# Kernel optimization log

Measured on AMD Instinct MI355X. Metric: run time of the kernel, lower is better.

The kernel has to match this reference:

```python
import jax, jax.numpy as jnp
import numpy as np

B, L, H, V = 256, 2048, 64, 64


def setup_inputs() -> dict:
    key = jax.random.key(0)
    ks = jax.random.split(key, 16)
    s = 0.05
    return {
        "seq": jax.random.randint(ks[0], (B, L), 0, V),
        "embed": jax.random.normal(ks[1], (V, H), jnp.float32) * s,
        "W1": jax.random.normal(ks[2], (2 * H, H), jnp.float32) * s,
        "b1": jnp.zeros((2 * H,), jnp.float32),
        "W2": jax.random.normal(ks[3], (H, 2 * H), jnp.float32) * s,
        "b2": jnp.zeros((H,), jnp.float32),
        "gamma": jnp.ones((H,), jnp.float32),
        "beta": jnp.zeros((H,), jnp.float32),
        "Wk": jax.random.normal(ks[4], (H, H), jnp.float32) * s,
        "Wv": jax.random.normal(ks[5], (H, H), jnp.float32) * s,
        "Wq": jax.random.normal(ks[6], (H, H), jnp.float32) * s,
        "Wrp": jax.random.normal(ks[7], (H, H), jnp.float32) * s,
        "brp": jnp.zeros((H,), jnp.float32),
        "Wout": jax.random.normal(ks[8], (V, H), jnp.float32) * s,
        "bout": jnp.zeros((V,), jnp.float32),
    }


def reference(seq, embed, W1, b1, W2, b2, gamma, beta, Wk, Wv, Wq, Wrp, brp, Wout, bout):
    # encode: LayerNorm(e + FF(e))
    e = embed[seq]                                   # [B, L, H]
    ff = jnp.maximum(e @ W1.T + b1, 0.0) @ W2.T + b2  # [B, L, H]
    h = e + ff
    mu = h.mean(-1, keepdims=True)
    var = ((h - mu) ** 2).mean(-1, keepdims=True)    # torch LN: biased var, eps=1e-5
    hs = (h - mu) / jnp.sqrt(var + 1e-5) * gamma + beta

    # precompute k/v for the first L-1 steps (batched GEMM)
    k_all = hs[:, :-1] @ Wk.T                         # [B, L-1, H]
    v_all = hs[:, :-1] @ Wv.T                         # [B, L-1, H]
    # F.normalize(k, dim=-1): k / max(||k||, 1e-12)
    k_n = k_all / jnp.maximum(jnp.linalg.norm(k_all, axis=-1, keepdims=True), 1e-12)

    def step(M, kv):
        k, v = kv                                      # each [B, H]
        vp = jnp.einsum('bij,bj->bi', M, k)
        M = M + jnp.einsum('bi,bj->bij', v - vp, k)    # rank-1 delta update
        return M, None

    M0 = jnp.zeros((B, H, H), hs.dtype)
    M, _ = jax.lax.scan(step, M0, (jnp.swapaxes(k_n, 0, 1), jnp.swapaxes(v_all, 0, 1)))

    q = hs[:, -1] @ Wq.T                               # [B, H]
    r = jnp.einsum('bij,bj->bi', M, q) @ Wrp.T + brp
    return r @ Wout.T + bout                           # [B, V]
```

## Files before the change

kernel.cpp:

```cpp
#include <hip/hip_runtime.h>


#define DPP_ADD_F32(x, ctrl, rm, bm, bc)                                      \
  (x) = (x) + __int_as_float(__builtin_amdgcn_update_dpp(                     \
            0, __float_as_int(x), (ctrl), (rm), (bm), (bc)))

__device__ __forceinline__ float wave_sum64(float x) {
  DPP_ADD_F32(x, 0x111, 0xf, 0xf, true);
  DPP_ADD_F32(x, 0x112, 0xf, 0xf, true);
  DPP_ADD_F32(x, 0x114, 0xf, 0xf, true);
  DPP_ADD_F32(x, 0x118, 0xf, 0xf, true);
  DPP_ADD_F32(x, 0x142, 0xa, 0xf, false);
  DPP_ADD_F32(x, 0x143, 0xc, 0xf, false);
  return __int_as_float(__builtin_amdgcn_readlane(__float_as_int(x), 63));
}

__device__ __forceinline__ float readlane_f(float x, int lane) {
  return __int_as_float(__builtin_amdgcn_readlane(__float_as_int(x), lane));
}

__global__ __launch_bounds__(64) void build_tables(
    const float* __restrict__ embed, const float* __restrict__ W1,
    const float* __restrict__ b1, const float* __restrict__ W2,
    const float* __restrict__ b2, const float* __restrict__ gamma,
    const float* __restrict__ beta, const float* __restrict__ Wk,
    const float* __restrict__ Wv, const float* __restrict__ Wq,
    float* __restrict__ k_tab, float* __restrict__ v_tab,
    float* __restrict__ q_tab) {
  __shared__ float Wbuf[8448];
  __shared__ float e_s[64];
  __shared__ float f1_s[128];
  __shared__ float hs_s[64];
  const int tok = blockIdx.x;
  const int l = threadIdx.x;

  const float e = embed[tok * 64 + l];
  e_s[l] = e;
  for (int i = 0; i < 128; ++i) Wbuf[i * 65 + l] = W1[i * 64 + l];
  __syncthreads();

  float a0 = b1[l], a1 = b1[l + 64];
#pragma unroll
  for (int h = 0; h < 64; ++h) {
    a0 = fmaf(e_s[h], Wbuf[l * 65 + h], a0);
    a1 = fmaf(e_s[h], Wbuf[(l + 64) * 65 + h], a1);
  }
  f1_s[l] = fmaxf(a0, 0.f);
  f1_s[l + 64] = fmaxf(a1, 0.f);
  __syncthreads();

  for (int i = 0; i < 128; ++i)
    Wbuf[(i >> 1) * 131 + (i & 1) * 64 + l] = W2[i * 64 + l];
  __syncthreads();

  float acc = b2[l];
#pragma unroll
  for (int j = 0; j < 128; ++j) acc = fmaf(f1_s[j], Wbuf[l * 131 + j], acc);
  const float hval = e + acc;

  const float mu = wave_sum64(hval) * (1.f / 64.f);
  const float d = hval - mu;
  const float var = wave_sum64(d * d) * (1.f / 64.f);
  const float hs = d * (1.f / sqrtf(var + 1e-5f)) * gamma[l] + beta[l];
  hs_s[l] = hs;
  __syncthreads();

  for (int i = 0; i < 64; ++i) {
    Wbuf[i * 65 + l] = Wk[i * 64 + l];
    Wbuf[4224 + i * 65 + l] = Wv[i * 64 + l];
  }
  __syncthreads();
  float kk = 0.f, vv = 0.f;
#pragma unroll
  for (int h = 0; h < 64; ++h) {
    kk = fmaf(hs_s[h], Wbuf[l * 65 + h], kk);
    vv = fmaf(hs_s[h], Wbuf[4224 + l * 65 + h], vv);
  }
  __syncthreads();
  for (int i = 0; i < 64; ++i) Wbuf[i * 65 + l] = Wq[i * 64 + l];
  __syncthreads();
  float qq = 0.f;
#pragma unroll
  for (int h = 0; h < 64; ++h) qq = fmaf(hs_s[h], Wbuf[l * 65 + h], qq);

  float nrm = fmaxf(sqrtf(wave_sum64(kk * kk)), 1e-12f);
  k_tab[tok * 64 + l] = kk / nrm;
  v_tab[tok * 64 + l] = vv;
  q_tab[tok * 64 + l] = qq;
}

__global__ __launch_bounds__(64) void build_gram(
    const float* __restrict__ k_tab, const float* __restrict__ q_tab,
    const float* __restrict__ v_tab, float2* __restrict__ GV,
    float* __restrict__ KQ) {
  __shared__ float k_s[4160];
  __shared__ float q_s[64];
  const int a = blockIdx.x;
  const int l = threadIdx.x;
  for (int i = 0; i < 64; ++i) k_s[i * 65 + l] = k_tab[i * 64 + l];
  q_s[l] = q_tab[a * 64 + l];
  __syncthreads();
  float g = 0.f, kq = 0.f;
#pragma unroll
  for (int h = 0; h < 64; ++h) {
    g = fmaf(k_s[a * 65 + h], k_s[l * 65 + h], g);
    kq = fmaf(q_s[h], k_s[l * 65 + h], kq);
  }
  GV[a * 64 + l] = make_float2(-g, v_tab[a * 64 + l]);
  KQ[a * 64 + l] = kq;
}

__global__ __launch_bounds__(256) void pack_tokens(const int* __restrict__ seq,
                                                   int* __restrict__ pk) {
  const int idx = blockIdx.x * 256 + threadIdx.x;
  const int b = idx / 410, w = idx - b * 410;
  const int* tp = seq + b * 2048;
  int acc = 0;
#pragma unroll
  for (int i = 0; i < 5; ++i) {
    const int j = 5 * w + 1 + i;
    const int t = (j <= 2047) ? tp[2047 - j] : 0;
    acc |= t << (6 * i);
  }
  pk[b * 412 + w] = acc;
}

__global__ __launch_bounds__(64, 1) void scan_head(
    const int* __restrict__ seq, const float2* __restrict__ GVg,
    const float* __restrict__ KQ, const int* __restrict__ pk,
    const float* __restrict__ Wrp, const float* __restrict__ brp,
    const float* __restrict__ Wout, const float* __restrict__ bout,
    float* __restrict__ out) {
  __shared__ float2 GV_s[4160];
  __shared__ int pk_s[448];
  __shared__ float tmp[64];
  const int b = blockIdx.x;
  const int l = threadIdx.x;

#pragma unroll
  for (int i = 0; i < 32; ++i)
    ((float4*)GV_s)[l + 64 * i] = ((const float4*)GVg)[l + 64 * i];
  const int* pkb = pk + b * 412;
#pragma unroll
  for (int i = 0; i < 7; ++i) {
    const int idx = l + 64 * i;
    pk_s[idx] = (idx < 410) ? pkb[idx] : 0;
  }
  __syncthreads();

  const int* tokp = seq + b * 2048;
  const int qt = tokp[2047];
  float y = KQ[qt * 64 + l];
  float r = 0.f;

  int S[5][5];
  int vw[5];
#pragma unroll
  for (int k = 0; k < 5; ++k) {
    const int u = __builtin_amdgcn_readfirstlane(pk_s[k]);
#pragma unroll
    for (int i = 0; i < 5; ++i) S[k][i] = (u >> (6 * i)) & 63;
  }
  vw[0] = pk_s[5];
  vw[1] = pk_s[6];
  vw[2] = 0;
  vw[3] = 0;
  vw[4] = 0;

  float2 c[25];
#pragma unroll
  for (int s = 0; s < 20; ++s) c[s] = GV_s[S[s / 5][s % 5] * 64 + l];

  for (int m = 0; m < 81; ++m) {
    const int wb = 5 * m;
#pragma unroll
    for (int q = 0; q < 5; ++q) {
      vw[(q + 2) % 5] = pk_s[wb + q + 7];
#pragma unroll
      for (int i = 0; i < 5; ++i) {
        const float2 gv = c[5 * q + i];
        c[(q == 0) ? (20 + i) : (5 * q - 5 + i)] =
            GV_s[S[(q + 4) % 5][i] * 64 + l];
        const float sv = readlane_f(y, S[q][i]);
        y = fmaf(sv, gv.x, y);
        r = fmaf(sv, gv.y, r);
      }
      const int u = __builtin_amdgcn_readfirstlane(vw[q]);
#pragma unroll
      for (int i = 0; i < 5; ++i) S[q][i] = (u >> (6 * i)) & 63;
    }
  }

#pragma unroll
  for (int q = 0; q < 4; ++q) {
#pragma unroll
    for (int i = 0; i < 5; ++i) {
      const float2 gv = c[5 * q + i];
      c[(q == 0) ? (20 + i) : (5 * q - 5 + i)] =
          GV_s[S[(q + 4) % 5][i] * 64 + l];
      const float sv = readlane_f(y, S[q][i]);
      y = fmaf(sv, gv.x, y);
      r = fmaf(sv, gv.y, r);
    }
  }
  {
    const float2 gv = c[20];
    const float sv = readlane_f(y, S[4][0]);
    y = fmaf(sv, gv.x, y);
    r = fmaf(sv, gv.y, r);
  }
  {
    const float2 gv = c[21];
    const float sv = readlane_f(y, S[4][1]);
    r = fmaf(sv, gv.y, r);
  }

  float* Wb = (float*)GV_s;
  tmp[l] = r;
  __syncthreads();
  for (int i = 0; i < 64; ++i) {
    Wb[i * 65 + l] = Wrp[i * 64 + l];
    Wb[4160 + i * 65 + l] = Wout[i * 64 + l];
  }
  __syncthreads();
  float acc = brp[l];
#pragma unroll
  for (int j = 0; j < 64; ++j) acc = fmaf(tmp[j], Wb[l * 65 + j], acc);
  __syncthreads();
  tmp[l] = acc;
  __syncthreads();
  float o = bout[l];
#pragma unroll
  for (int i = 0; i < 64; ++i) o = fmaf(tmp[i], Wb[4160 + l * 65 + i], o);
  out[b * 64 + l] = o;
}

extern "C" void kernel_launch(void* const* d_in, const int* in_sizes, int n_in,
                              void* d_out, int out_size, void* d_ws,
                              size_t ws_size, hipStream_t stream) {
  const int* seq = (const int*)d_in[0];
  const float* embed = (const float*)d_in[1];
  const float* W1 = (const float*)d_in[2];
  const float* b1 = (const float*)d_in[3];
  const float* W2 = (const float*)d_in[4];
  const float* b2 = (const float*)d_in[5];
  const float* gamma = (const float*)d_in[6];
  const float* beta = (const float*)d_in[7];
  const float* Wk = (const float*)d_in[8];
  const float* Wv = (const float*)d_in[9];
  const float* Wq = (const float*)d_in[10];
  const float* Wrp = (const float*)d_in[11];
  const float* brp = (const float*)d_in[12];
  const float* Wout = (const float*)d_in[13];
  const float* bout = (const float*)d_in[14];

  float* wsf = (float*)d_ws;
  float* k_tab = wsf;
  float* v_tab = wsf + 4096;
  float* q_tab = wsf + 8192;
  float2* GV = (float2*)(wsf + 12288);
  float* KQ = wsf + 20480;
  int* pk = (int*)(wsf + 24576);

  build_tables<<<64, 64, 0, stream>>>(embed, W1, b1, W2, b2, gamma, beta, Wk,
                                      Wv, Wq, k_tab, v_tab, q_tab);
  build_gram<<<64, 64, 0, stream>>>(k_tab, q_tab, v_tab, GV, KQ);
  pack_tokens<<<410, 256, 0, stream>>>(seq, pk);
  scan_head<<<256, 64, 0, stream>>>(seq, GV, KQ, pk, Wrp, brp, Wout, bout,
                                    (float*)d_out);
}
```

Before: 148.3 us.

## Break serial scan dependency by deferring y updates with precomputed scalar coefficients

Restructures the backward scan so each step's scalar is computed from a lagged readlane plus a 3-term correction using precomputed Gram coefficients between nearby tokens. The vector update of y is applied three steps late, so the readlane→fma→readlane chain no longer serialises on every step. This adds a per-block precompute pass that fills a coefficient table in shared memory, plus extra scalar FMAs per step, and it raises LDS use, which risks occupancy and correctness at the sequence boundaries.

```diff
diff --git a/kernel.cpp b/kernel.cpp
--- a/kernel.cpp
+++ b/kernel.cpp
@@ -125,6 +125,33 @@
   pk[b * 412 + w] = acc;
 }
 
+#define PHASE(P, P5, CFc, CFn)                                                \
+  {                                                                           \
+    const int JB_ = 5 * (P) + 1;                                              \
+    _Pragma("unroll") for (int i5 = 0; i5 < 5; ++i5) CFn[i5] =                \
+        coef_s[JB_ + 5 + i5];                                                 \
+    vwr[((P5) % 5 + 2) % 5] = pk_s[(P) + 7];                                  \
+    _Pragma("unroll") for (int i5 = 0; i5 < 5; ++i5) {                        \
+      const float pj = readlane_f(y, S[(P5) % 5][i5]);                        \
+      const float2 cY = c[(5 * (P5) + i5 + 7) % 10];                          \
+      c[(5 * (P5) + i5 + 5) % 10] =                                           \
+          GV_s[S[((P5) % 5 + 1) % 5][i5] * 64 + l];                           \
+      y = fmaf(s3, cY.x, y);                                                  \
+      r = fmaf(s3, cY.y, r);                                                  \
+      const float4 cf_ = CFc[i5];                                             \
+      const float sj_ =                                                       \
+          fmaf(cf_.x, s1, fmaf(cf_.y, s2, fmaf(cf_.z, s3, pj)));              \
+      s3 = s2;                                                                \
+      s2 = s1;                                                                \
+      s1 = sj_;                                                               \
+    }                                                                         \
+    {                                                                         \
+      const int u_ = __builtin_amdgcn_readfirstlane(vwr[(P5) % 5]);           \
+      _Pragma("unroll") for (int i5 = 0; i5 < 5; ++i5) S[(P5) % 5][i5] =      \
+          (u_ >> (6 * i5)) & 63;                                              \
+    }                                                                         \
+  }
+
 __global__ __launch_bounds__(64, 1) void scan_head(
     const int* __restrict__ seq, const float2* __restrict__ GVg,
     const float* __restrict__ KQ, const int* __restrict__ pk,
@@ -132,6 +159,7 @@
     const float* __restrict__ Wout, const float* __restrict__ bout,
     float* __restrict__ out) {
   __shared__ float2 GV_s[4160];
+  __shared__ float4 coef_s[2064];
   __shared__ int pk_s[448];
   __shared__ float tmp[64];
   const int b = blockIdx.x;
@@ -140,6 +168,7 @@
 #pragma unroll
   for (int i = 0; i < 32; ++i)
     ((float4*)GV_s)[l + 64 * i] = ((const float4*)GVg)[l + 64 * i];
+  GV_s[4096 + l] = make_float2(0.f, 0.f);
   const int* pkb = pk + b * 412;
 #pragma unroll
   for (int i = 0; i < 7; ++i) {
@@ -149,71 +178,101 @@
   __syncthreads();
 
   const int* tokp = seq + b * 2048;
+
+  for (int it = 0; it < 32; ++it) {
+    const int j = it * 64 + l;
+    float c1 = 0.f, c2 = 0.f, c3 = 0.f;
+    if (j >= 1) {
+      const int t0 = tokp[2047 - j];
+      const int t1 = (j >= 2) ? tokp[2048 - j] : 64;
+      const int t2 = (j >= 3) ? tokp[2049 - j] : 64;
+      const int t3 = (j >= 4) ? tokp[2050 - j] : 64;
+      if (t1 < 64) c1 = GV_s[t0 * 64 + t1].x;
+      if (t2 < 64) c2 = GV_s[t0 * 64 + t2].x;
+      if (t3 < 64) c3 = GV_s[t0 * 64 + t3].x;
+    }
+    coef_s[j] = make_float4(c1, c2, c3, 0.f);
+  }
+  if (l < 16) coef_s[2048 + l] = make_float4(0.f, 0.f, 0.f, 0.f);
+  __syncthreads();
+
   const int qt = tokp[2047];
   float y = KQ[qt * 64 + l];
   float r = 0.f;
+  float s1 = 0.f, s2 = 0.f, s3 = 0.f;
 
   int S[5][5];
-  int vw[5];
+  int vwr[5];
 #pragma unroll
   for (int k = 0; k < 5; ++k) {
     const int u = __builtin_amdgcn_readfirstlane(pk_s[k]);
 #pragma unroll
     for (int i = 0; i < 5; ++i) S[k][i] = (u >> (6 * i)) & 63;
   }
-  vw[0] = pk_s[5];
-  vw[1] = pk_s[6];
-  vw[2] = 0;
-  vw[3] = 0;
-  vw[4] = 0;
-
-  float2 c[25];
-#pragma unroll
-  for (int s = 0; s < 20; ++s) c[s] = GV_s[S[s / 5][s % 5] * 64 + l];
-
-  for (int m = 0; m < 81; ++m) {
-    const int wb = 5 * m;
-#pragma unroll
-    for (int q = 0; q < 5; ++q) {
-      vw[(q + 2) % 5] = pk_s[wb + q + 7];
-#pragma unroll
-      for (int i = 0; i < 5; ++i) {
-        const float2 gv = c[5 * q + i];
-        c[(q == 0) ? (20 + i) : (5 * q - 5 + i)] =
-            GV_s[S[(q + 4) % 5][i] * 64 + l];
-        const float sv = readlane_f(y, S[q][i]);
-        y = fmaf(sv, gv.x, y);
-        r = fmaf(sv, gv.y, r);
-      }
-      const int u = __builtin_amdgcn_readfirstlane(vw[q]);
-#pragma unroll
-      for (int i = 0; i < 5; ++i) S[q][i] = (u >> (6 * i)) & 63;
-    }
-  }
-
-#pragma unroll
-  for (int q = 0; q < 4; ++q) {
-#pragma unroll
-    for (int i = 0; i < 5; ++i) {
-      const float2 gv = c[5 * q + i];
-      c[(q == 0) ? (20 + i) : (5 * q - 5 + i)] =
-          GV_s[S[(q + 4) % 5][i] * 64 + l];
-      const float sv = readlane_f(y, S[q][i]);
-      y = fmaf(sv, gv.x, y);
-      r = fmaf(sv, gv.y, r);
-    }
-  }
+  vwr[0] = pk_s[5];
+  vwr[1] = pk_s[6];
+  vwr[2] = 0;
+  vwr[3] = 0;
+  vwr[4] = 0;
+
+  float2 c[10];
+  c[7] = make_float2(0.f, 0.f);
+  c[8] = make_float2(0.f, 0.f);
+  c[9] = make_float2(0.f, 0.f);
+#pragma unroll
+  for (int i = 0; i < 5; ++i) c[i] = GV_s[S[0][i] * 64 + l];
+
+  float4 cfA[5], cfB[5];
+#pragma unroll
+  for (int i = 0; i < 5; ++i) cfA[i] = coef_s[1 + i];
+
+  for (int MM = 0; MM < 40; ++MM) {
+    const int P0 = 10 * MM;
+    PHASE(P0 + 0, 0, cfA, cfB);
+    PHASE(P0 + 1, 1, cfB, cfA);
+    PHASE(P0 + 2, 2, cfA, cfB);
+    PHASE(P0 + 3, 3, cfB, cfA);
+    PHASE(P0 + 4, 4, cfA, cfB);
+    PHASE(P0 + 5, 5, cfB, cfA);
+    PHASE(P0 + 6, 6, cfA, cfB);
+    PHASE(P0 + 7, 7, cfB, cfA);
+    PHASE(P0 + 8, 8, cfA, cfB);
+    PHASE(P0 + 9, 9, cfB, cfA);
+  }
+  PHASE(400, 0, cfA, cfB);
+  PHASE(401, 1, cfB, cfA);
+  PHASE(402, 2, cfA, cfB);
+  PHASE(403, 3, cfB, cfA);
+  PHASE(404, 4, cfA, cfB);
+  PHASE(405, 5, cfB, cfA);
+  PHASE(406, 6, cfA, cfB);
+  PHASE(407, 7, cfB, cfA);
+  PHASE(408, 8, cfA, cfB);
+
   {
-    const float2 gv = c[20];
-    const float sv = readlane_f(y, S[4][0]);
-    y = fmaf(sv, gv.x, y);
-    r = fmaf(sv, gv.y, r);
+    const float p0 = readlane_f(y, S[4][0]);
+    const float2 cY0 = c[2];
+    y = fmaf(s3, cY0.x, y);
+    r = fmaf(s3, cY0.y, r);
+    const float4 cf0 = cfB[0];
+    const float sj0 = fmaf(cf0.x, s1, fmaf(cf0.y, s2, fmaf(cf0.z, s3, p0)));
+    s3 = s2;
+    s2 = s1;
+    s1 = sj0;
   }
   {
-    const float2 gv = c[21];
-    const float sv = readlane_f(y, S[4][1]);
-    r = fmaf(sv, gv.y, r);
-  }
+    const float p1 = readlane_f(y, S[4][1]);
+    const float2 cY1 = c[3];
+    r = fmaf(s3, cY1.y, r);
+    const float4 cf1 = cfB[1];
+    const float sj1 = fmaf(cf1.x, s1, fmaf(cf1.y, s2, fmaf(cf1.z, s3, p1)));
+    s3 = s2;
+    s2 = s1;
+    s1 = sj1;
+  }
+  r = fmaf(s3, c[4].y, r);
+  r = fmaf(s2, c[5].y, r);
+  r = fmaf(s1, c[6].y, r);
 
   float* Wb = (float*)GV_s;
   tmp[l] = r;
```

Measured after the change: 180.6 us. +21.8%, slower.
